# Performance work log

Measured on AMD Instinct MI355X. Metric: run time of the kernel, lower is better.

Reference implementation:

```python
import jax, jax.numpy as jnp
import numpy as np

T = 500_000  # sequence length
K = 16       # number of hidden states


def setup_inputs() -> dict:
    key = jax.random.key(0)
    k1, k2, k3, k4 = jax.random.split(key, 4)
    y = jax.random.normal(k1, (T,), dtype=jnp.float32)
    transition_logits = jax.random.normal(k2, (K, K), dtype=jnp.float32)
    mu = 2.0 * jax.random.normal(k3, (K,), dtype=jnp.float32)
    log_sigma = 0.1 * jax.random.normal(k4, (K,), dtype=jnp.float32)
    return {"y": y, "transition_logits": transition_logits, "mu": mu, "log_sigma": log_sigma}


def _stationary_distribution(P):
    # Solve pi P = pi, sum(pi) = 1 via least squares (normal equations: differentiable, jit-safe).
    k = P.shape[0]
    A = jnp.concatenate([P.T - jnp.eye(k, dtype=P.dtype), jnp.ones((1, k), dtype=P.dtype)], axis=0)
    b = jnp.concatenate([jnp.zeros((k,), dtype=P.dtype), jnp.ones((1,), dtype=P.dtype)])
    return jnp.linalg.solve(A.T @ A, A.T @ b)


def reference(y, transition_logits, mu, log_sigma):
    P = jax.nn.softmax(transition_logits, axis=-1)  # [K, K] row-stochastic transition matrix
    sigma = jnp.exp(log_sigma)
    # Gaussian emission densities g[t, k] = N(y_t; mu_k, sigma_k^2)
    z = (y[:, None] - mu[None, :]) / sigma[None, :]
    INV_SQRT_2PI = 0.3989422804014327
    g = jnp.exp(-0.5 * z * z) * (INV_SQRT_2PI / sigma)[None, :]  # [T, K]

    ut0 = _stationary_distribution(P)              # [K]
    g0 = g[0]
    ft0 = jnp.sum(ut0 * g0)                        # scalar
    utt0 = ut0 * g0 / ft0                          # [K]

    def step(utt_prev, gt):
        ut = utt_prev @ P                          # predictive dist [K]
        ft = jnp.sum(ut * gt)                      # normalizer
        utt = ut * gt / ft                         # filtered posterior [K]
        return utt, (ut, ft, utt)

    _, (Ut, ft_rest, Utt) = jax.lax.scan(step, utt0, g[1:])

    ut = jnp.concatenate([ut0[None, :], Ut], axis=0)       # [T, K]
    u_norm = jnp.concatenate([utt0[None, :], Utt], axis=0)  # [T, K]
    ft = jnp.concatenate([ft0[None], ft_rest], axis=0)      # [T]
    return (ut, u_norm, ft)
```

## Files before the change

kernel.cpp:

```cpp
#include <hip/hip_runtime.h>

#define CHUNK_L 32
#define WARMUP_W 16

typedef float v2f __attribute__((ext_vector_type(2)));

template<int K> __device__ __forceinline__ float bcast16(float v) {
    return __int_as_float(__builtin_amdgcn_update_dpp(
        0, __float_as_int(v), 0x150 | K, 0xF, 0xF, true));
}
template<int N> __device__ __forceinline__ float rowror16(float v) {
    return __int_as_float(__builtin_amdgcn_update_dpp(
        0, __float_as_int(v), 0x120 | N, 0xF, 0xF, true));
}

__device__ __forceinline__ float rowsum16(float p) {
    p += rowror16<1>(p);
    p += rowror16<2>(p);
    p += rowror16<4>(p);
    p += rowror16<8>(p);
    return p;
}

__device__ __forceinline__ float dot16(float a, const v2f* pc2) {
    v2f b0, b1, u01, u23;
    b0.x = bcast16<0>(a);  b0.y = bcast16<1>(a);
    b1.x = bcast16<2>(a);  b1.y = bcast16<3>(a);
    u01 = b0 * pc2[0];
    u23 = b1 * pc2[1];
    b0.x = bcast16<4>(a);  b0.y = bcast16<5>(a);
    b1.x = bcast16<6>(a);  b1.y = bcast16<7>(a);
    u01 = b0 * pc2[2] + u01;
    u23 = b1 * pc2[3] + u23;
    b0.x = bcast16<8>(a);  b0.y = bcast16<9>(a);
    b1.x = bcast16<10>(a); b1.y = bcast16<11>(a);
    u01 = b0 * pc2[4] + u01;
    u23 = b1 * pc2[5] + u23;
    b0.x = bcast16<12>(a); b0.y = bcast16<13>(a);
    b1.x = bcast16<14>(a); b1.y = bcast16<15>(a);
    u01 = b0 * pc2[6] + u01;
    u23 = b1 * pc2[7] + u23;
    v2f u = u01 + u23;
    return u.x + u.y;
}

__global__ __launch_bounds__(256, 4) void hmm_filter_kernel(
    const float* __restrict__ y,
    const float* __restrict__ logits,
    const float* __restrict__ mu,
    const float* __restrict__ log_sigma,
    float* __restrict__ out,
    int T, int nchunks)
{
    __shared__ float Plds[256];
    __shared__ float Ba[256];
    __shared__ float Bb[256];

    const int tid = (int)threadIdx.x;
    const int j   = tid & 15;
    const int g   = tid >> 4;

    float l = logits[tid];
    float m = l;
    #pragma unroll
    for (int s = 1; s < 16; s <<= 1) m = fmaxf(m, __shfl_xor(m, s, 16));
    float e = __expf(l - m);
    float rs = e;
    #pragma unroll
    for (int s = 1; s < 16; s <<= 1) rs += __shfl_xor(rs, s, 16);
    float Pv = e / rs;
    Plds[tid] = Pv;
    Ba[tid]   = Pv;
    __syncthreads();

    float* cur = Ba;
    float* nxt = Bb;
    for (int itq = 0; itq < 10; ++itq) {
        float acc = 0.f;
        #pragma unroll
        for (int k = 0; k < 16; ++k)
            acc += cur[g * 16 + k] * cur[k * 16 + j];
        float rsum = acc;
        #pragma unroll
        for (int s = 1; s < 16; s <<= 1) rsum += __shfl_xor(rsum, s, 16);
        nxt[tid] = acc / rsum;
        __syncthreads();
        float* tmp = cur; cur = nxt; nxt = tmp;
    }

    const float api = cur[j];

    v2f pc2[8];
    #pragma unroll
    for (int k = 0; k < 8; ++k) {
        pc2[k].x = Plds[(2 * k)     * 16 + j];
        pc2[k].y = Plds[(2 * k + 1) * 16 + j];
    }

    const float muj = mu[j];
    const float isj = __expf(-log_sigma[j]);
    const float nmj = -muj * isj;
    const float lcf = __log2f(0.3989422804014327f * isj);
    const float K2  = -0.7213475204444817f;

    const int chunk = (int)blockIdx.x * 16 + g;
    if (chunk >= nchunks) return;

    const int wfrom = chunk * CHUNK_L;
    int t0 = wfrom - WARMUP_W; if (t0 < 0) t0 = 0;
    const int nwb = (wfrom - t0) >> 2;
    const int Tm4 = T - 4;
    const int TN  = T << 4;

    auto emis = [&](float yt) -> float {
        float z = fmaf(yt, isj, nmj);
        return __builtin_amdgcn_exp2f(fmaf(z * z, K2, lcf));
    };

    float p = api;
    int t = t0;

    float4 c4 = *(const float4*)(y + t);
    int pf = t + 4; if (pf > Tm4) pf = Tm4;
    float4 n1 = *(const float4*)(y + pf);

    for (int b = 0; b < nwb; ++b) {
        int p2 = t + 8; if (p2 > Tm4) p2 = Tm4;
        const float4 n2 = *(const float4*)(y + p2);
        p = dot16(p, pc2) * emis(c4.x);
        p = dot16(p, pc2) * emis(c4.y);
        p = dot16(p, pc2) * emis(c4.z);
        p = dot16(p, pc2) * emis(c4.w);
        if (b == 1) p *= __builtin_amdgcn_rcpf(rowsum16(p));
        c4 = n1; n1 = n2; t += 4;
    }
    p *= __builtin_amdgcn_rcpf(rowsum16(p));

    float* __restrict__ pU = out + (wfrom << 4) + j;
    float* __restrict__ pN = pU + TN;
    float* __restrict__ pF = out + 2 * TN + wfrom;

    #pragma unroll 1
    for (int b = 0; b < (CHUNK_L / 4); ++b) {
        int p2 = t + 8; if (p2 > Tm4) p2 = Tm4;
        const float4 n2 = *(const float4*)(y + p2);

        const float q0  = dot16(p, pc2);
        const float pg0 = q0 * emis(c4.x);
        const float s0  = rowsum16(pg0);
        const float r0  = __builtin_amdgcn_rcpf(s0);
        const float q1  = dot16(pg0, pc2);
        const float pg1 = q1 * emis(c4.y);
        const float s1  = rowsum16(pg1);
        const float r1  = __builtin_amdgcn_rcpf(s1);
        const float q2  = dot16(pg1, pc2);
        const float pg2 = q2 * emis(c4.z);
        const float s2  = rowsum16(pg2);
        const float r2  = __builtin_amdgcn_rcpf(s2);
        const float q3  = dot16(pg2, pc2);
        const float pg3 = q3 * emis(c4.w);
        const float s3  = rowsum16(pg3);
        const float r3  = __builtin_amdgcn_rcpf(s3);

        pU[0]  = q0;
        pU[16] = q1 * r0;
        pU[32] = q2 * r1;
        pU[48] = q3 * r2;
        pN[0]  = pg0 * r0;
        pN[16] = pg1 * r1;
        pN[32] = pg2 * r2;
        const float utt3 = pg3 * r3;
        pN[48] = utt3;
        if (j == 0)
            *(float4*)pF = make_float4(s0, s1 * r0, s2 * r1, s3 * r2);

        p = utt3;
        pU += 64; pN += 64; pF += 4;
        c4 = n1; n1 = n2; t += 4;
    }
}

extern "C" void kernel_launch(void* const* d_in, const int* in_sizes, int n_in,
                              void* d_out, int out_size, void* d_ws, size_t ws_size,
                              hipStream_t stream) {
    const float* y      = (const float*)d_in[0];
    const float* logits = (const float*)d_in[1];
    const float* mu     = (const float*)d_in[2];
    const float* ls     = (const float*)d_in[3];
    float* out = (float*)d_out;
    const int T = in_sizes[0];

    const int nchunks = (T + CHUNK_L - 1) / CHUNK_L;
    const int blocks  = (nchunks + 15) / 16;
    hmm_filter_kernel<<<blocks, 256, 0, stream>>>(y, logits, mu, ls, out,
                                                  T, nchunks);
}
```

Baseline: 95.44 us.

## Preload y window into registers, fully unroll, and replace LDS matrix squaring with power iteration

The stationary distribution is now computed per thread by 48 register-resident power-iteration steps using the existing DPP dot product. This replaces 10 rounds of LDS-based matrix squaring separated by block barriers, and the Ba/Bb shared buffers go away. Each chunk now loads its whole 48-sample y window into registers up front and fully unrolls both the warmup and the main loops, so the rolling prefetch and clamp logic is gone. The softmax also switches to DPP row max/sum with exp2/rcp. The price is a longer serial dependency chain for the stationary vector and more registers held live. The removed clamps assume T is a multiple of the chunk length.

```diff
diff --git a/kernel.cpp b/kernel.cpp
--- a/kernel.cpp
+++ b/kernel.cpp
@@ -2,6 +2,7 @@
 
 #define CHUNK_L 32
 #define WARMUP_W 16
+#define PI_ITERS 48
 
 typedef float v2f __attribute__((ext_vector_type(2)));
 
@@ -13,12 +14,18 @@
     return __int_as_float(__builtin_amdgcn_update_dpp(
         0, __float_as_int(v), 0x120 | N, 0xF, 0xF, true));
 }
-
 __device__ __forceinline__ float rowsum16(float p) {
     p += rowror16<1>(p);
     p += rowror16<2>(p);
     p += rowror16<4>(p);
     p += rowror16<8>(p);
+    return p;
+}
+__device__ __forceinline__ float rowmax16(float p) {
+    p = fmaxf(p, rowror16<1>(p));
+    p = fmaxf(p, rowror16<2>(p));
+    p = fmaxf(p, rowror16<4>(p));
+    p = fmaxf(p, rowror16<8>(p));
     return p;
 }
 
@@ -53,42 +60,17 @@
     int T, int nchunks)
 {
     __shared__ float Plds[256];
-    __shared__ float Ba[256];
-    __shared__ float Bb[256];
 
     const int tid = (int)threadIdx.x;
     const int j   = tid & 15;
     const int g   = tid >> 4;
 
-    float l = logits[tid];
-    float m = l;
-    #pragma unroll
-    for (int s = 1; s < 16; s <<= 1) m = fmaxf(m, __shfl_xor(m, s, 16));
-    float e = __expf(l - m);
-    float rs = e;
-    #pragma unroll
-    for (int s = 1; s < 16; s <<= 1) rs += __shfl_xor(rs, s, 16);
-    float Pv = e / rs;
+    const float l  = logits[tid];
+    const float mx = rowmax16(l);
+    const float e  = __builtin_amdgcn_exp2f((l - mx) * 1.4426950408889634f);
+    const float Pv = e * __builtin_amdgcn_rcpf(rowsum16(e));
     Plds[tid] = Pv;
-    Ba[tid]   = Pv;
     __syncthreads();
-
-    float* cur = Ba;
-    float* nxt = Bb;
-    for (int itq = 0; itq < 10; ++itq) {
-        float acc = 0.f;
-        #pragma unroll
-        for (int k = 0; k < 16; ++k)
-            acc += cur[g * 16 + k] * cur[k * 16 + j];
-        float rsum = acc;
-        #pragma unroll
-        for (int s = 1; s < 16; s <<= 1) rsum += __shfl_xor(rsum, s, 16);
-        nxt[tid] = acc / rsum;
-        __syncthreads();
-        float* tmp = cur; cur = nxt; nxt = tmp;
-    }
-
-    const float api = cur[j];
 
     v2f pc2[8];
     #pragma unroll
@@ -97,86 +79,90 @@
         pc2[k].y = Plds[(2 * k + 1) * 16 + j];
     }
 
-    const float muj = mu[j];
-    const float isj = __expf(-log_sigma[j]);
-    const float nmj = -muj * isj;
-    const float lcf = __log2f(0.3989422804014327f * isj);
-    const float K2  = -0.7213475204444817f;
-
     const int chunk = (int)blockIdx.x * 16 + g;
     if (chunk >= nchunks) return;
 
-    const int wfrom = chunk * CHUNK_L;
-    int t0 = wfrom - WARMUP_W; if (t0 < 0) t0 = 0;
-    const int nwb = (wfrom - t0) >> 2;
-    const int Tm4 = T - 4;
-    const int TN  = T << 4;
+    float api = 0.0625f;
+    #pragma unroll
+    for (int i = 0; i < PI_ITERS; ++i) api = dot16(api, pc2);
+    api *= __builtin_amdgcn_rcpf(rowsum16(api));
 
+    const float isj = __expf(-log_sigma[j]);
+    const float nmj = -mu[j] * isj;
+    const float lcf = __log2f(0.3989422804014327f * isj);
+    const float K2  = -0.7213475204444817f;
     auto emis = [&](float yt) -> float {
         float z = fmaf(yt, isj, nmj);
         return __builtin_amdgcn_exp2f(fmaf(z * z, K2, lcf));
     };
 
+    const int wfrom = chunk * CHUNK_L;
+    int t0 = wfrom - WARMUP_W; if (t0 < 0) t0 = 0;
+    const bool first = (wfrom == 0);
+
+    const float4* yb = (const float4*)(y + t0);
+    float4 Y[12];
+    #pragma unroll
+    for (int i = 0; i < 12; ++i) Y[i] = yb[i];
+
     float p = api;
-    int t = t0;
-
-    float4 c4 = *(const float4*)(y + t);
-    int pf = t + 4; if (pf > Tm4) pf = Tm4;
-    float4 n1 = *(const float4*)(y + pf);
-
-    for (int b = 0; b < nwb; ++b) {
-        int p2 = t + 8; if (p2 > Tm4) p2 = Tm4;
-        const float4 n2 = *(const float4*)(y + p2);
+    #pragma unroll
+    for (int i = 0; i < 4; ++i) {
+        const float4 c4 = Y[i];
         p = dot16(p, pc2) * emis(c4.x);
         p = dot16(p, pc2) * emis(c4.y);
         p = dot16(p, pc2) * emis(c4.z);
         p = dot16(p, pc2) * emis(c4.w);
-        if (b == 1) p *= __builtin_amdgcn_rcpf(rowsum16(p));
-        c4 = n1; n1 = n2; t += 4;
+        if (i == 1) p *= __builtin_amdgcn_rcpf(rowsum16(p));
     }
     p *= __builtin_amdgcn_rcpf(rowsum16(p));
+    if (first) p = api;
+
+    float4 M[8];
+    #pragma unroll
+    for (int i = 0; i < 8; ++i) M[i] = first ? Y[i] : Y[i + 4];
 
     float* __restrict__ pU = out + (wfrom << 4) + j;
-    float* __restrict__ pN = pU + TN;
-    float* __restrict__ pF = out + 2 * TN + wfrom;
+    float* __restrict__ pN = pU + (T << 4);
+    float* __restrict__ pF = out + (T << 5) + wfrom;
 
-    #pragma unroll 1
-    for (int b = 0; b < (CHUNK_L / 4); ++b) {
-        int p2 = t + 8; if (p2 > Tm4) p2 = Tm4;
-        const float4 n2 = *(const float4*)(y + p2);
+    #pragma unroll
+    for (int b = 0; b < 8; ++b) {
+        const float4 c4 = M[b];
+        const float g0 = emis(c4.x), g1 = emis(c4.y);
+        const float g2 = emis(c4.z), g3 = emis(c4.w);
 
         const float q0  = dot16(p, pc2);
-        const float pg0 = q0 * emis(c4.x);
+        const float pg0 = q0 * g0;
         const float s0  = rowsum16(pg0);
         const float r0  = __builtin_amdgcn_rcpf(s0);
         const float q1  = dot16(pg0, pc2);
-        const float pg1 = q1 * emis(c4.y);
+        const float pg1 = q1 * g1;
         const float s1  = rowsum16(pg1);
         const float r1  = __builtin_amdgcn_rcpf(s1);
         const float q2  = dot16(pg1, pc2);
-        const float pg2 = q2 * emis(c4.z);
+        const float pg2 = q2 * g2;
         const float s2  = rowsum16(pg2);
         const float r2  = __builtin_amdgcn_rcpf(s2);
         const float q3  = dot16(pg2, pc2);
-        const float pg3 = q3 * emis(c4.w);
+        const float pg3 = q3 * g3;
         const float s3  = rowsum16(pg3);
         const float r3  = __builtin_amdgcn_rcpf(s3);
 
-        pU[0]  = q0;
-        pU[16] = q1 * r0;
-        pU[32] = q2 * r1;
-        pU[48] = q3 * r2;
-        pN[0]  = pg0 * r0;
-        pN[16] = pg1 * r1;
-        pN[32] = pg2 * r2;
+        const int o = b * 64;
+        pU[o]      = q0;
+        pU[o + 16] = q1 * r0;
+        pU[o + 32] = q2 * r1;
+        pU[o + 48] = q3 * r2;
+        pN[o]      = pg0 * r0;
+        pN[o + 16] = pg1 * r1;
+        pN[o + 32] = pg2 * r2;
         const float utt3 = pg3 * r3;
-        pN[48] = utt3;
+        pN[o + 48] = utt3;
         if (j == 0)
-            *(float4*)pF = make_float4(s0, s1 * r0, s2 * r1, s3 * r2);
+            *(float4*)(pF + b * 4) = make_float4(s0, s1 * r0, s2 * r1, s3 * r2);
 
         p = utt3;
-        pU += 64; pN += 64; pF += 4;
-        c4 = n1; n1 = n2; t += 4;
     }
 }
 
```

Measured after the change: 98.07 us. 1.03x slower.
